# Optimization experiments

Measured on AMD Instinct MI355X. Metric: run time of the kernel, lower is better.

## Reference

```python
import jax, jax.numpy as jnp
import numpy as np

EPS = 1e-8


def cos_loss(a, b):
    # a, b: [n, c, h, w]; cosine distance over channel dim, mean over rest
    a_norm = jnp.sqrt((a * a).sum(1, keepdims=True))
    b_norm = jnp.sqrt((b * b).sum(1, keepdims=True))
    cossim = ((a / (a_norm + EPS)) * (b / (b_norm + EPS))).sum(1)
    return (1.0 - cossim).mean()


def nn_feat_replace(a, b):
    # a: [1, c, h, w], b: [1, c, h2, w2]
    n, c, h, w = a.shape
    a_flat = a.reshape(n, c, -1)                    # [1, c, hw]
    b_flat = b.reshape(n, c, -1)                    # [1, c, h2w2]
    # normalize along channel dim (matches argmin_cos_distance's two-eps scheme)
    b_n = b_flat / (jnp.sqrt((b_flat * b_flat).sum(1, keepdims=True) + EPS) + EPS)
    a_n = a_flat / (jnp.sqrt((a_flat * a_flat).sum(1, keepdims=True) + EPS) + EPS)
    # full cosine-distance matrix: [1, hw, h2w2]
    d_mat = 1.0 - jnp.einsum('bci,bcj->bij', a_n, b_n)
    z_best = jnp.argmin(d_mat, axis=2)              # [1, hw]
    feat = jnp.take(b_flat, z_best[0], axis=2)      # gather: [1, c, hw]
    return feat.reshape(n, c, h, w)


def setup_inputs() -> dict:
    key = jax.random.key(0)
    k1, k2 = jax.random.split(key)
    a = jax.random.normal(k1, (1, 768, 128, 128), dtype=jnp.float32)
    b = jax.random.normal(k2, (1, 768, 128, 128), dtype=jnp.float32)
    return {"a": a, "b": b}


def reference(a, b):
    target = nn_feat_replace(a, b)
    return cos_loss(a, target)
```

## Files before the change

### kernel.cpp

```cpp
#include <hip/hip_runtime.h>
#include <stdint.h>

#define HW 16384
#define CDIM 768
#define EPSF 1e-8f

typedef float f32x4  __attribute__((ext_vector_type(4)));
typedef float f32x16 __attribute__((ext_vector_type(16)));
typedef int   i32x8  __attribute__((ext_vector_type(8)));
typedef uint32_t u32x4 __attribute__((ext_vector_type(4)));

__device__ inline void async16(const void* g, void* l) {
    __builtin_amdgcn_global_load_lds(
        (const __attribute__((address_space(1))) uint32_t*)g,
        (__attribute__((address_space(3))) uint32_t*)l, 16, 0, 0);
}

__device__ inline uint32_t pk4_fp8(float v0, float v1, float v2, float v3) {
    uint32_t r = __builtin_amdgcn_cvt_pk_fp8_f32(v0, v1, 0, false);
    r = __builtin_amdgcn_cvt_pk_fp8_f32(v2, v3, r, true);
    return r;
}

__global__ void __launch_bounds__(256)
transpose_fp8_norm(const float* __restrict__ a, const float* __restrict__ b,
                   uint8_t* __restrict__ at8, uint8_t* __restrict__ bn8,
                   float* __restrict__ sumsq_a, float* __restrict__ sumsq_b) {
    const int z = blockIdx.z;
    const float* src = z ? b : a;
    uint8_t* dst = z ? bn8 : at8;
    float* sums = z ? sumsq_b : sumsq_a;
    const float mult = z ? 8.0f : 16.0f;

    __shared__ float tile[64][65];
    const int s0 = blockIdx.x * 64, c0 = blockIdx.y * 64;
    const int tx = threadIdx.x & 63, ty = threadIdx.x >> 6;
#pragma unroll
    for (int p = 0; p < 16; ++p) {
        int cl = p * 4 + ty;
        tile[cl][tx] = src[(size_t)(c0 + cl) * HW + s0 + tx];
    }
    __syncthreads();

    const int chgrp = tx & 15, rowsub = tx >> 4;
    uint32_t* dst32 = (uint32_t*)dst;
#pragma unroll
    for (int p = 0; p < 4; ++p) {
        int sl = p * 16 + ty * 4 + rowsub;
        float v0 = tile[chgrp * 4 + 0][sl];
        float v1 = tile[chgrp * 4 + 1][sl];
        float v2 = tile[chgrp * 4 + 2][sl];
        float v3 = tile[chgrp * 4 + 3][sl];
        float part = v0 * v0 + v1 * v1 + v2 * v2 + v3 * v3;
        dst32[(size_t)(s0 + sl) * (CDIM / 4) + (c0 >> 2) + chgrp] =
            pk4_fp8(v0 * mult, v1 * mult, v2 * mult, v3 * mult);
#pragma unroll
        for (int m = 1; m < 16; m <<= 1) part += __shfl_xor(part, m, 64);
        if (chgrp == 0) atomicAdd(&sums[s0 + sl], part);
    }
}

__global__ void prep_invd(const float* __restrict__ sumsq_b,
                          float* __restrict__ invdb) {
    int j = blockIdx.x * 256 + threadIdx.x;
    invdb[j] = 1.0f / (sqrtf(sumsq_b[j] + EPSF) + EPSF);
}

__global__ void __launch_bounds__(256, 2)
gemm_argmax(const uint8_t* __restrict__ at8, const uint8_t* __restrict__ bn8,
            const float* __restrict__ invdb,
            unsigned long long* __restrict__ best) {
    __shared__ uint8_t Al[2 * 16384];
    __shared__ uint8_t Bl[2 * 8192];

    const int g = blockIdx.x;
    const int xcd    = g & 7;
    const int s      = g >> 3;
    const int super  = s >> 5;
    const int within = s & 31;
    const int si = super >> 4;
    const int sj = super & 15;
    const int it = xcd * 8 + si * 4 + (within & 3);
    const int jt = sj * 8 + (within >> 2);

    const int i0 = it * 256, j0 = jt * 128;
    const int tid = threadIdx.x;
    const int lane = tid & 63, w = tid >> 6;
    const int wi = w & 1, wj = w >> 1;
    const int l31 = lane & 31, hi = lane >> 5;

    f32x16 acc[2][4] = {};

    const int srow = lane >> 2;
    const int schunk = ((lane & 3) ^ ((lane >> 3) & 3)) * 16;
    const uint8_t* gA = at8 + (size_t)(i0 + w * 64 + srow) * CDIM + schunk;
    const uint8_t* gB = bn8 + (size_t)(j0 + w * 32 + srow) * CDIM + schunk;
    uint8_t* lA = Al + w * 4096;
    uint8_t* lB = Bl + w * 2048;

    const int rA0 = (wi * 128 + l31) * 64;
    const int rB0 = (wj * 64 + l31) * 64;
    const int c0 = ((hi * 2) ^ ((l31 >> 1) & 3)) * 16;

#define STAGE(boA, boB, kk)                                    \
    do {                                                       \
        async16(gA + (kk),             lA + (boA));            \
        async16(gA + (kk) + 16 * CDIM, lA + (boA) + 1024);     \
        async16(gA + (kk) + 32 * CDIM, lA + (boA) + 2048);     \
        async16(gA + (kk) + 48 * CDIM, lA + (boA) + 3072);     \
        async16(gB + (kk),             lB + (boB));            \
        async16(gB + (kk) + 16 * CDIM, lB + (boB) + 1024);     \
    } while (0)

#define COMPUTE(boA, boB)                                                    \
    do {                                                                     \
        i32x8 af0, af1, af2, af3, bg;                                        \
        *(u32x4*)&af0       = *(const u32x4*)&Al[(boA) + rA0 + c0];          \
        *((u32x4*)&af0 + 1) = *(const u32x4*)&Al[(boA) + rA0 + (c0 ^ 16)];   \
        *(u32x4*)&af1       = *(const u32x4*)&Al[(boA) + rA0 + 2048 + c0];   \
        *((u32x4*)&af1 + 1) = *(const u32x4*)&Al[(boA) + rA0 + 2048 + (c0 ^ 16)]; \
        *(u32x4*)&af2       = *(const u32x4*)&Al[(boA) + rA0 + 4096 + c0];   \
        *((u32x4*)&af2 + 1) = *(const u32x4*)&Al[(boA) + rA0 + 4096 + (c0 ^ 16)]; \
        *(u32x4*)&af3       = *(const u32x4*)&Al[(boA) + rA0 + 6144 + c0];   \
        *((u32x4*)&af3 + 1) = *(const u32x4*)&Al[(boA) + rA0 + 6144 + (c0 ^ 16)]; \
        *(u32x4*)&bg        = *(const u32x4*)&Bl[(boB) + rB0 + c0];          \
        *((u32x4*)&bg + 1)  = *(const u32x4*)&Bl[(boB) + rB0 + (c0 ^ 16)];   \
        acc[0][0] = __builtin_amdgcn_mfma_scale_f32_32x32x64_f8f6f4(         \
            bg, af0, acc[0][0], 0, 0, 0, 0x7F7F7F7F, 0, 0x7F7F7F7F);         \
        acc[0][1] = __builtin_amdgcn_mfma_scale_f32_32x32x64_f8f6f4(         \
            bg, af1, acc[0][1], 0, 0, 0, 0x7F7F7F7F, 0, 0x7F7F7F7F);         \
        acc[0][2] = __builtin_amdgcn_mfma_scale_f32_32x32x64_f8f6f4(         \
            bg, af2, acc[0][2], 0, 0, 0, 0x7F7F7F7F, 0, 0x7F7F7F7F);         \
        acc[0][3] = __builtin_amdgcn_mfma_scale_f32_32x32x64_f8f6f4(         \
            bg, af3, acc[0][3], 0, 0, 0, 0x7F7F7F7F, 0, 0x7F7F7F7F);         \
        *(u32x4*)&bg        = *(const u32x4*)&Bl[(boB) + rB0 + 2048 + c0];   \
        *((u32x4*)&bg + 1)  = *(const u32x4*)&Bl[(boB) + rB0 + 2048 + (c0 ^ 16)]; \
        acc[1][0] = __builtin_amdgcn_mfma_scale_f32_32x32x64_f8f6f4(         \
            bg, af0, acc[1][0], 0, 0, 0, 0x7F7F7F7F, 0, 0x7F7F7F7F);         \
        acc[1][1] = __builtin_amdgcn_mfma_scale_f32_32x32x64_f8f6f4(         \
            bg, af1, acc[1][1], 0, 0, 0, 0x7F7F7F7F, 0, 0x7F7F7F7F);         \
        acc[1][2] = __builtin_amdgcn_mfma_scale_f32_32x32x64_f8f6f4(         \
            bg, af2, acc[1][2], 0, 0, 0, 0x7F7F7F7F, 0, 0x7F7F7F7F);         \
        acc[1][3] = __builtin_amdgcn_mfma_scale_f32_32x32x64_f8f6f4(         \
            bg, af3, acc[1][3], 0, 0, 0, 0x7F7F7F7F, 0, 0x7F7F7F7F);         \
    } while (0)

    STAGE(0, 0, 0);
    asm volatile("s_waitcnt vmcnt(0)" ::: "memory");
    __builtin_amdgcn_s_barrier();

#pragma unroll 1
    for (int t = 0; t < 11; ++t) {
        const int boA = (t & 1) * 16384, boB = (t & 1) * 8192;
        STAGE(boA ^ 16384, boB ^ 8192, (t + 1) * 64);
        COMPUTE(boA, boB);
        asm volatile("s_waitcnt vmcnt(0)" ::: "memory");
        __builtin_amdgcn_s_barrier();
    }
    COMPUTE(16384, 8192);

#undef STAGE
#undef COMPUTE

    float bv[4] = {-1e30f, -1e30f, -1e30f, -1e30f};
    int   bj[4] = {0, 0, 0, 0};
#pragma unroll
    for (int nj = 0; nj < 2; ++nj) {
        const int jb = j0 + wj * 64 + nj * 32 + 4 * hi;
        f32x4 iv[4];
#pragma unroll
        for (int q = 0; q < 4; ++q)
            iv[q] = *(const f32x4*)&invdb[jb + 8 * q];
#pragma unroll
        for (int mi = 0; mi < 4; ++mi) {
#pragma unroll
            for (int r = 0; r < 16; ++r) {
                int j = jb + (r & 3) + 8 * (r >> 2);
                float v = acc[nj][mi][r] * iv[r >> 2][r & 3];
                if (v > bv[mi] || (v == bv[mi] && j < bj[mi])) {
                    bv[mi] = v; bj[mi] = j;
                }
            }
        }
    }
#pragma unroll
    for (int mi = 0; mi < 4; ++mi) {
        float ov = __shfl_xor(bv[mi], 32, 64);
        int   oj = __shfl_xor(bj[mi], 32, 64);
        if (ov > bv[mi] || (ov == bv[mi] && oj < bj[mi])) {
            bv[mi] = ov; bj[mi] = oj;
        }
        if (hi == 0) {
            int gi = i0 + wi * 128 + mi * 32 + l31;
            uint32_t u = __float_as_uint(bv[mi]);
            u = (u & 0x80000000u) ? ~u : (u | 0x80000000u);
            unsigned long long packed =
                ((unsigned long long)u << 32) | (uint32_t)(~(uint32_t)bj[mi]);
            atomicMax(&best[gi], packed);
        }
    }
}

__global__ void loss_reduce(const unsigned long long* __restrict__ best,
                            const float* __restrict__ sumsq_a,
                            const float* __restrict__ sumsq_b,
                            float* __restrict__ out) {
    int i = blockIdx.x * 256 + threadIdx.x;
    unsigned long long pk = best[i];
    uint32_t x = (uint32_t)(pk >> 32);
    float v = (x & 0x80000000u) ? __uint_as_float(x & 0x7fffffffu)
                                : __uint_as_float(~x);
    int j = (int)(~(uint32_t)pk);
    float sb = sumsq_b[j];
    float denb = sqrtf(sb + EPSF) + EPSF;
    float dot = v * denb * (1.0f / 128.0f);
    float cs = dot / ((sqrtf(sumsq_a[i]) + EPSF) * (sqrtf(sb) + EPSF));
    float term = 1.0f - cs;
#pragma unroll
    for (int m = 32; m; m >>= 1) term += __shfl_down(term, m, 64);
    __shared__ float red[4];
    int wv = threadIdx.x >> 6, lane = threadIdx.x & 63;
    if (lane == 0) red[wv] = term;
    __syncthreads();
    if (threadIdx.x == 0) {
        float ssum = (red[0] + red[1] + red[2] + red[3]) * (1.0f / HW);
        atomicAdd(out, ssum);
    }
}

extern "C" void kernel_launch(void* const* d_in, const int* in_sizes, int n_in,
                              void* d_out, int out_size, void* d_ws, size_t ws_size,
                              hipStream_t stream) {
    const float* a = (const float*)d_in[0];
    const float* b = (const float*)d_in[1];
    char* ws = (char*)d_ws;

    const size_t T_BYTES = (size_t)HW * CDIM;
    uint8_t* at8 = (uint8_t*)ws;
    uint8_t* bn8 = (uint8_t*)(ws + T_BYTES);
    float* sumsq_a = (float*)(ws + 2 * T_BYTES);
    float* sumsq_b = (float*)(ws + 2 * T_BYTES + HW * sizeof(float));
    unsigned long long* best =
        (unsigned long long*)(ws + 2 * T_BYTES + 2 * HW * sizeof(float));
    float* invdb = (float*)(ws + 2 * T_BYTES + 2 * HW * sizeof(float)
                            + HW * sizeof(unsigned long long));

    hipMemsetAsync(sumsq_a, 0, 2 * HW * sizeof(float) + HW * sizeof(unsigned long long),
                   stream);
    hipMemsetAsync(d_out, 0, out_size * sizeof(float), stream);

    dim3 tg(HW / 64, CDIM / 64, 2);
    transpose_fp8_norm<<<tg, 256, 0, stream>>>(a, b, at8, bn8, sumsq_a, sumsq_b);
    prep_invd<<<HW / 256, 256, 0, stream>>>(sumsq_b, invdb);
    gemm_argmax<<<(HW / 256) * (HW / 128), 256, 0, stream>>>(at8, bn8, invdb, best);
    loss_reduce<<<HW / 256, 256, 0, stream>>>(best, sumsq_a, sumsq_b, (float*)d_out);
}
```

Before: 432.1 us.

## Triple-buffer LDS staging in fp8 GEMM-argmax and raise MFMA wave priority

Moves the GEMM main loop from double to triple buffering of the A/B tiles in LDS. Two K-chunks are kept in flight, and each wait uses a partial vmcnt instead of draining all loads. s_setprio is also raised around the MFMA block so compute waves get scheduler priority. The aim is to hide global-to-LDS load latency behind the matrix ops. In exchange LDS use rises to 72KB per block, which may reduce occupancy below the two blocks per CU the launch bounds assume.

```diff
diff --git a/kernel.cpp b/kernel.cpp
--- a/kernel.cpp
+++ b/kernel.cpp
@@ -70,8 +70,8 @@
 gemm_argmax(const uint8_t* __restrict__ at8, const uint8_t* __restrict__ bn8,
             const float* __restrict__ invdb,
             unsigned long long* __restrict__ best) {
-    __shared__ uint8_t Al[2 * 16384];
-    __shared__ uint8_t Bl[2 * 8192];
+    __shared__ uint8_t Al[3 * 16384];
+    __shared__ uint8_t Bl[3 * 8192];
 
     const int g = blockIdx.x;
     const int xcd    = g & 7;
@@ -125,6 +125,7 @@
         *((u32x4*)&af3 + 1) = *(const u32x4*)&Al[(boA) + rA0 + 6144 + (c0 ^ 16)]; \
         *(u32x4*)&bg        = *(const u32x4*)&Bl[(boB) + rB0 + c0];          \
         *((u32x4*)&bg + 1)  = *(const u32x4*)&Bl[(boB) + rB0 + (c0 ^ 16)];   \
+        __builtin_amdgcn_s_setprio(1);                                       \
         acc[0][0] = __builtin_amdgcn_mfma_scale_f32_32x32x64_f8f6f4(         \
             bg, af0, acc[0][0], 0, 0, 0, 0x7F7F7F7F, 0, 0x7F7F7F7F);         \
         acc[0][1] = __builtin_amdgcn_mfma_scale_f32_32x32x64_f8f6f4(         \
@@ -143,24 +144,44 @@
             bg, af2, acc[1][2], 0, 0, 0, 0x7F7F7F7F, 0, 0x7F7F7F7F);         \
         acc[1][3] = __builtin_amdgcn_mfma_scale_f32_32x32x64_f8f6f4(         \
             bg, af3, acc[1][3], 0, 0, 0, 0x7F7F7F7F, 0, 0x7F7F7F7F);         \
+        __builtin_amdgcn_s_setprio(0);                                       \
     } while (0)
 
+#define WAITN(n) asm volatile("s_waitcnt vmcnt(" #n ")" ::: "memory")
+
     STAGE(0, 0, 0);
-    asm volatile("s_waitcnt vmcnt(0)" ::: "memory");
+    STAGE(16384, 8192, 64);
+
+#pragma unroll 1
+    for (int r = 0; r < 3; ++r) {
+        const int t0 = r * 3;
+        WAITN(6);
+        __builtin_amdgcn_s_barrier();
+        STAGE(2 * 16384, 2 * 8192, (t0 + 2) * 64);
+        COMPUTE(0, 0);
+        WAITN(6);
+        __builtin_amdgcn_s_barrier();
+        STAGE(0, 0, (t0 + 3) * 64);
+        COMPUTE(16384, 8192);
+        WAITN(6);
+        __builtin_amdgcn_s_barrier();
+        STAGE(16384, 8192, (t0 + 4) * 64);
+        COMPUTE(2 * 16384, 2 * 8192);
+    }
+    WAITN(6);
     __builtin_amdgcn_s_barrier();
-
-#pragma unroll 1
-    for (int t = 0; t < 11; ++t) {
-        const int boA = (t & 1) * 16384, boB = (t & 1) * 8192;
-        STAGE(boA ^ 16384, boB ^ 8192, (t + 1) * 64);
-        COMPUTE(boA, boB);
-        asm volatile("s_waitcnt vmcnt(0)" ::: "memory");
-        __builtin_amdgcn_s_barrier();
-    }
+    STAGE(2 * 16384, 2 * 8192, 11 * 64);
+    COMPUTE(0, 0);
+    WAITN(6);
+    __builtin_amdgcn_s_barrier();
     COMPUTE(16384, 8192);
+    WAITN(0);
+    __builtin_amdgcn_s_barrier();
+    COMPUTE(2 * 16384, 2 * 8192);
 
 #undef STAGE
 #undef COMPUTE
+#undef WAITN
 
     float bv[4] = {-1e30f, -1e30f, -1e30f, -1e30f};
     int   bj[4] = {0, 0, 0, 0};
```

Result: slower. 487.2 us (+12.8%).
